# Optimization experiments

Measured on AMD Instinct MI355X. Metric: run time of the kernel, lower is better.

Reference implementation:

```python
import jax, jax.numpy as jnp
import numpy as np


def _conv2d(x, w, b):
    # x: [N,C,H,W], w: [O,I,kh,kw], valid conv, stride 1 (matches nn.Conv2d defaults)
    y = jax.lax.conv_general_dilated(
        x, w, window_strides=(1, 1), padding='VALID',
        dimension_numbers=('NCHW', 'OIHW', 'NCHW'))
    return y + b[None, :, None, None]


def _max_pool2(x):
    # F.max_pool2d(x, 2): 2x2 window, stride 2, no padding
    return jax.lax.reduce_window(
        x, -jnp.inf, jax.lax.max,
        window_dimensions=(1, 1, 2, 2), window_strides=(1, 1, 2, 2),
        padding='VALID')


def setup_inputs() -> dict:
    key = jax.random.key(0)
    ks = jax.random.split(key, 12)
    B = 16384
    def w(k, shape, fan_in):
        bound = 1.0 / np.sqrt(fan_in)
        return jax.random.uniform(k, shape, jnp.float32, -bound, bound)
    return {
        'x': jax.random.normal(ks[0], (B, 1, 28, 28), jnp.float32),
        'conv1_w': w(ks[1], (8, 1, 3, 3), 1 * 9),
        'conv1_b': w(ks[2], (8,), 1 * 9),
        'conv2_w': w(ks[3], (16, 8, 3, 3), 8 * 9),
        'conv2_b': w(ks[4], (16,), 8 * 9),
        'fc_w': w(ks[5], (128, 400), 400),
        'fc_b': w(ks[6], (128,), 400),
        'fc2_w': w(ks[7], (64, 128), 128),
        'fc2_b': w(ks[8], (64,), 128),
        'fc3_w': w(ks[9], (10, 64), 64),
        'fc3_b': w(ks[10], (10,), 64),
    }


def reference(x, conv1_w, conv1_b, conv2_w, conv2_b,
              fc_w, fc_b, fc2_w, fc2_b, fc3_w, fc3_b):
    out = jax.nn.relu(_conv2d(x, conv1_w, conv1_b))          # [B,8,26,26]
    out = _max_pool2(out)                                    # [B,8,13,13]
    out = jax.nn.relu(_conv2d(out, conv2_w, conv2_b))        # [B,16,11,11]
    out = _max_pool2(out)                                    # [B,16,5,5]
    out = out.reshape(out.shape[0], -1)                      # [B,400] (C,H,W order)
    out = jax.nn.relu(out @ fc_w.T + fc_b)                   # [B,128]
    out = out @ fc2_w.T + fc2_b                              # [B,64]
    out = out @ fc3_w.T + fc3_b                              # [B,10]
    return out
```

## Files before the change

kernel.cpp:

```cpp
#include <hip/hip_runtime.h>
#include <hip/hip_bf16.h>

typedef _Float16 half8 __attribute__((ext_vector_type(8)));
typedef float floatx4 __attribute__((ext_vector_type(4)));

__global__ __launch_bounds__(512, 4) void lenet_mfma(
    const float* __restrict__ X,
    const float* __restrict__ W1, const float* __restrict__ B1,
    const float* __restrict__ W2, const float* __restrict__ B2,
    const float* __restrict__ FW, const float* __restrict__ FB,
    const float* __restrict__ F2W, const float* __restrict__ F2B,
    const float* __restrict__ F3W, const float* __restrict__ F3B,
    float* __restrict__ OUT) {
  __shared__ __align__(16) _Float16 p2h[32 * 416];
  __shared__ __align__(16) char p1region[10816];
  __shared__ __align__(16) char region[20480];
  __shared__ __align__(16) _Float16 w2L[16 * 104];
  __shared__ float w1L[72];
  __shared__ float bc1L[8], bc2L[16], fbL[128], f2bL[64], f3bL[16];
  __shared__ __align__(16) _Float16 zero16[8];

  float* xs = (float*)region;
  _Float16* c2f = (_Float16*)region;
  _Float16* fwdb = (_Float16*)region;
  _Float16* w2sf = (_Float16*)region;
  float* w3sf = (float*)(region + 17408);
  _Float16* p1f = (_Float16*)p1region;
  float* h2f = (float*)p1region;
  _Float16* h1f = p2h;

  const int tid = threadIdx.x;
  const int wave = tid >> 6;
  const int lane = tid & 63;
  const int l15 = lane & 15;
  const int l4 = lane >> 4;
  const int m32 = blockIdx.x * 32;

  for (int i = tid; i < 72; i += 512) w1L[i] = W1[i];
  if (tid < 8) bc1L[tid] = B1[tid];
  if (tid >= 8 && tid < 24) bc2L[tid - 8] = B2[tid - 8];
  if (tid >= 32 && tid < 160) fbL[tid - 32] = FB[tid - 32];
  if (tid >= 160 && tid < 224) f2bL[tid - 160] = F2B[tid - 160];
  if (tid >= 224 && tid < 234) f3bL[tid - 224] = F3B[tid - 224];
  if (tid >= 240 && tid < 248) zero16[tid - 240] = (_Float16)0.f;
  for (int i = tid; i < 16 * 104; i += 512) {
    int oc = i / 104, k = i % 104;
    _Float16 v = (_Float16)0.f;
    if (k < 72) { int tap = k >> 3, ic = k & 7; v = (_Float16)W2[(oc * 8 + ic) * 9 + tap]; }
    w2L[i] = v;
  }
  if (tid < 512) { int rr = tid >> 4, cc = tid & 15; p2h[rr * 416 + 400 + cc] = (_Float16)0.f; }
  for (int i = tid; i < 784; i += 512) {
    int m = i / 196, f = i % 196;
    ((float4*)(xs + m * 784))[f] = ((const float4*)(X + (size_t)(m32 + m) * 784))[f];
  }
  __syncthreads();

  half8 bw0 = *(const half8*)(w2L + l15 * 104 + 0 + l4 * 8);
  half8 bw1 = *(const half8*)(w2L + l15 * 104 + 32 + l4 * 8);
  half8 bw2 = *(const half8*)(w2L + l15 * 104 + 64 + l4 * 8);
  int off0, off1, off2; int va0, va1, va2;
  {
    int tap, du, dv;
    tap = 0 * 4 + l4; du = (tap >= 6) ? 2 : ((tap >= 3) ? 1 : 0); dv = tap - 3 * du;
    off0 = (du * 13 + dv) * 16; va0 = (tap < 9);
    tap = 1 * 4 + l4; du = (tap >= 6) ? 2 : ((tap >= 3) ? 1 : 0); dv = tap - 3 * du;
    off1 = (du * 13 + dv) * 16; va1 = (tap < 9);
    tap = 2 * 4 + l4; du = (tap >= 6) ? 2 : ((tap >= 3) ? 1 : 0); dv = tap - 3 * du;
    off2 = (du * 13 + dv) * 16; va2 = (tap < 9);
  }

  for (int sb = 0; sb < 8; ++sb) {
    for (int t = tid; t < 416; t += 512) {
      int ch = t & 7, rm = t >> 3, m = rm / 13, r = rm % 13;
      float wk[9];
#pragma unroll
      for (int k = 0; k < 9; k++) wk[k] = w1L[ch * 9 + k];
      float b = bc1L[ch];
      const float* Xb = xs + m * 784 + 2 * r * 28;
      float2 A0[4], A1[4];
#pragma unroll
      for (int row = 0; row < 4; row++) {
        A0[row] = *(const float2*)(Xb + row * 28);
        A1[row] = *(const float2*)(Xb + row * 28 + 2);
      }
#pragma unroll
      for (int c = 0; c < 13; c++) {
        if (c) {
#pragma unroll
          for (int row = 0; row < 4; row++) {
            A0[row] = A1[row];
            A1[row] = *(const float2*)(Xb + row * 28 + 2 * c + 2);
          }
        }
        float s0 = 0.f, s1 = 0.f, s2 = 0.f, s3 = 0.f;
#pragma unroll
        for (int u = 0; u < 3; u++) {
          float w0 = wk[u * 3], w1 = wk[u * 3 + 1], w2v = wk[u * 3 + 2];
          float xu0 = A0[u].x, xu1 = A0[u].y, xu2 = A1[u].x, xu3 = A1[u].y;
          s0 += w0 * xu0 + w1 * xu1 + w2v * xu2;
          s1 += w0 * xu1 + w1 * xu2 + w2v * xu3;
          float xd0 = A0[u + 1].x, xd1 = A0[u + 1].y, xd2 = A1[u + 1].x, xd3 = A1[u + 1].y;
          s2 += w0 * xd0 + w1 * xd1 + w2v * xd2;
          s3 += w0 * xd1 + w1 * xd2 + w2v * xd3;
        }
        float mx = fmaxf(fmaxf(s0, s1), fmaxf(s2, s3));
        p1f[((m * 13 + r) * 13 + c) * 8 + ch] = (_Float16)fmaxf(mx + b, 0.f);
      }
    }
    __syncthreads();

    for (int mt = wave; mt < 31; mt += 8) {
      int p = mt * 16 + l15; if (p > 483) p = 483;
      int img = p / 121, rem = p - img * 121;
      int r = rem / 11, c = rem - r * 11;
      int base = ((img * 13 + r) * 13 + c) * 16;
      const char* p1c = (const char*)p1f;
      floatx4 acc = {0.f, 0.f, 0.f, 0.f};
      half8 a0 = *(const half8*)(va0 ? (p1c + base + off0) : (const char*)zero16);
      acc = __builtin_amdgcn_mfma_f32_16x16x32_f16(a0, bw0, acc, 0, 0, 0);
      half8 a1 = *(const half8*)(va1 ? (p1c + base + off1) : (const char*)zero16);
      acc = __builtin_amdgcn_mfma_f32_16x16x32_f16(a1, bw1, acc, 0, 0, 0);
      half8 a2 = *(const half8*)(va2 ? (p1c + base + off2) : (const char*)zero16);
      acc = __builtin_amdgcn_mfma_f32_16x16x32_f16(a2, bw2, acc, 0, 0, 0);
      int pb = mt * 16 + l4 * 4;
#pragma unroll
      for (int rr = 0; rr < 4; rr++) {
        int pos = pb + rr;
        if (pos < 484) c2f[pos * 16 + l15] = (_Float16)acc[rr];
      }
    }
    __syncthreads();

    for (int t = tid; t < 1600; t += 512) {
      int oc = t & 15, q = t >> 4;
      int m = q / 25, rc = q % 25, r = rc / 5, cc = rc % 5;
      int p00 = m * 121 + (2 * r) * 11 + 2 * cc;
      float v00 = (float)c2f[p00 * 16 + oc];
      float v01 = (float)c2f[(p00 + 1) * 16 + oc];
      float v10 = (float)c2f[(p00 + 11) * 16 + oc];
      float v11 = (float)c2f[(p00 + 12) * 16 + oc];
      float mx = fmaxf(fmaxf(v00, v01), fmaxf(v10, v11));
      p2h[(sb * 4 + m) * 416 + oc * 25 + r * 5 + cc] = (_Float16)fmaxf(mx + bc2L[oc], 0.f);
    }
    __syncthreads();
    if (sb < 7) {
      for (int i = tid; i < 784; i += 512) {
        int m = i / 196, f = i % 196;
        ((float4*)(xs + m * 784))[f] =
            ((const float4*)(X + (size_t)(m32 + (sb + 1) * 4 + m) * 784))[f];
      }
    }
    __syncthreads();
  }

  const int so = tid >> 2, sq = tid & 3;
  auto stageFW = [&](int c, int buf) {
    int kk = c * 32 + sq * 8;
    float4 z = {0.f, 0.f, 0.f, 0.f};
    float4 v0 = (kk < 400) ? *(const float4*)(FW + (size_t)so * 400 + kk) : z;
    float4 v1 = (kk + 4 < 400) ? *(const float4*)(FW + (size_t)so * 400 + kk + 4) : z;
    half8 h = {(_Float16)v0.x, (_Float16)v0.y, (_Float16)v0.z, (_Float16)v0.w,
               (_Float16)v1.x, (_Float16)v1.y, (_Float16)v1.z, (_Float16)v1.w};
    *(half8*)(fwdb + buf * 5120 + so * 40 + sq * 8) = h;
  };
  stageFW(0, 0);
  const int mt1 = wave & 1, nt0 = wave >> 1;
  floatx4 acc0 = {0.f, 0.f, 0.f, 0.f}, acc1 = {0.f, 0.f, 0.f, 0.f};
  for (int c = 0; c < 13; ++c) {
    __syncthreads();
    if (c < 12) stageFW(c + 1, (c + 1) & 1);
    const _Float16* fb = fwdb + (c & 1) * 5120;
    half8 a = *(const half8*)(p2h + (mt1 * 16 + l15) * 416 + c * 32 + l4 * 8);
    half8 b0 = *(const half8*)(fb + (nt0 * 16 + l15) * 40 + l4 * 8);
    half8 b1 = *(const half8*)(fb + ((nt0 + 4) * 16 + l15) * 40 + l4 * 8);
    acc0 = __builtin_amdgcn_mfma_f32_16x16x32_f16(a, b0, acc0, 0, 0, 0);
    acc1 = __builtin_amdgcn_mfma_f32_16x16x32_f16(a, b1, acc1, 0, 0, 0);
  }
  __syncthreads();

  {
    float bias0 = fbL[nt0 * 16 + l15], bias1 = fbL[(nt0 + 4) * 16 + l15];
#pragma unroll
    for (int rr = 0; rr < 4; rr++) {
      int img = mt1 * 16 + l4 * 4 + rr;
      h1f[img * 136 + nt0 * 16 + l15] = (_Float16)fmaxf(acc0[rr] + bias0, 0.f);
      h1f[img * 136 + (nt0 + 4) * 16 + l15] = (_Float16)fmaxf(acc1[rr] + bias1, 0.f);
    }
  }
  {
    int o = tid >> 3, q = tid & 7;
    const float* src = F2W + (size_t)o * 128 + q * 16;
    float4 v0 = *(const float4*)(src);
    float4 v1 = *(const float4*)(src + 4);
    float4 v2 = *(const float4*)(src + 8);
    float4 v3 = *(const float4*)(src + 12);
    half8 hA = {(_Float16)v0.x, (_Float16)v0.y, (_Float16)v0.z, (_Float16)v0.w,
                (_Float16)v1.x, (_Float16)v1.y, (_Float16)v1.z, (_Float16)v1.w};
    half8 hB = {(_Float16)v2.x, (_Float16)v2.y, (_Float16)v2.z, (_Float16)v2.w,
                (_Float16)v3.x, (_Float16)v3.y, (_Float16)v3.z, (_Float16)v3.w};
    *(half8*)(w2sf + o * 136 + q * 16) = hA;
    *(half8*)(w2sf + o * 136 + q * 16 + 8) = hB;
  }
  for (int i = tid; i < 640; i += 512) w3sf[(i >> 6) * 68 + (i & 63)] = F3W[i];
  __syncthreads();

  {
    floatx4 acc2 = {0.f, 0.f, 0.f, 0.f};
#pragma unroll
    for (int kt = 0; kt < 4; kt++) {
      half8 a = *(const half8*)(h1f + (mt1 * 16 + l15) * 136 + kt * 32 + l4 * 8);
      half8 b = *(const half8*)(w2sf + (nt0 * 16 + l15) * 136 + kt * 32 + l4 * 8);
      acc2 = __builtin_amdgcn_mfma_f32_16x16x32_f16(a, b, acc2, 0, 0, 0);
    }
    float b2v = f2bL[nt0 * 16 + l15];
#pragma unroll
    for (int rr = 0; rr < 4; rr++) {
      int img = mt1 * 16 + l4 * 4 + rr;
      h2f[img * 68 + nt0 * 16 + l15] = acc2[rr] + b2v;
    }
  }
  __syncthreads();

  {
    int img = tid >> 4, o = tid & 15;
    if (o < 10) {
      float s = f3bL[o];
#pragma unroll
      for (int k4 = 0; k4 < 16; k4++) {
        float4 hv = *(const float4*)(h2f + img * 68 + k4 * 4);
        float4 wv = *(const float4*)(w3sf + o * 68 + k4 * 4);
        s += hv.x * wv.x + hv.y * wv.y + hv.z * wv.z + hv.w * wv.w;
      }
      OUT[(size_t)(m32 + img) * 10 + o] = s;
    }
  }
}

extern "C" void kernel_launch(void* const* d_in, const int* in_sizes, int n_in,
                              void* d_out, int out_size, void* d_ws, size_t ws_size,
                              hipStream_t stream) {
  const float* x   = (const float*)d_in[0];
  const float* c1w = (const float*)d_in[1];
  const float* c1b = (const float*)d_in[2];
  const float* c2w = (const float*)d_in[3];
  const float* c2b = (const float*)d_in[4];
  const float* fw  = (const float*)d_in[5];
  const float* fb  = (const float*)d_in[6];
  const float* f2w = (const float*)d_in[7];
  const float* f2b = (const float*)d_in[8];
  const float* f3w = (const float*)d_in[9];
  const float* f3b = (const float*)d_in[10];
  float* out = (float*)d_out;

  const int B = in_sizes[0] / 784;
  lenet_mfma<<<B / 32, 512, 0, stream>>>(x, c1w, c1b, c2w, c2b,
                                         fw, fb, f2w, f2b, f3w, f3b, out);
}
```

Baseline: 153.6 us.

## Move conv1 to MFMA, fuse pools into conv epilogues, halve images per block

After: 136.2 us. -11.3%, faster.

```diff
diff --git a/kernel.cpp b/kernel.cpp
--- a/kernel.cpp
+++ b/kernel.cpp
@@ -4,7 +4,7 @@
 typedef _Float16 half8 __attribute__((ext_vector_type(8)));
 typedef float floatx4 __attribute__((ext_vector_type(4)));
 
-__global__ __launch_bounds__(512, 4) void lenet_mfma(
+__global__ __launch_bounds__(512, 8) void lenet_mfma2(
     const float* __restrict__ X,
     const float* __restrict__ W1, const float* __restrict__ B1,
     const float* __restrict__ W2, const float* __restrict__ B2,
@@ -12,54 +12,65 @@
     const float* __restrict__ F2W, const float* __restrict__ F2B,
     const float* __restrict__ F3W, const float* __restrict__ F3B,
     float* __restrict__ OUT) {
-  __shared__ __align__(16) _Float16 p2h[32 * 416];
-  __shared__ __align__(16) char p1region[10816];
-  __shared__ __align__(16) char region[20480];
+  __shared__ __align__(16) _Float16 p2h[16 * 424];
+  __shared__ __align__(16) char region[18944];
   __shared__ __align__(16) _Float16 w2L[16 * 104];
-  __shared__ float w1L[72];
+  __shared__ __align__(16) _Float16 c1B[1280];
   __shared__ float bc1L[8], bc2L[16], fbL[128], f2bL[64], f3bL[16];
   __shared__ __align__(16) _Float16 zero16[8];
 
-  float* xs = (float*)region;
-  _Float16* c2f = (_Float16*)region;
-  _Float16* fwdb = (_Float16*)region;
+  _Float16* xs = (_Float16*)region;
+  _Float16* p1f = (_Float16*)(region + 7168);
   _Float16* w2sf = (_Float16*)region;
-  float* w3sf = (float*)(region + 17408);
-  _Float16* p1f = (_Float16*)p1region;
-  float* h2f = (float*)p1region;
+  _Float16* w3sf = (_Float16*)(region + 17408);
   _Float16* h1f = p2h;
+  float* h2f = (float*)((char*)p2h + 6656);
 
   const int tid = threadIdx.x;
-  const int wave = tid >> 6;
-  const int lane = tid & 63;
-  const int l15 = lane & 15;
-  const int l4 = lane >> 4;
-  const int m32 = blockIdx.x * 32;
-
-  for (int i = tid; i < 72; i += 512) w1L[i] = W1[i];
+  const int wave = tid >> 6, lane = tid & 63, l15 = lane & 15, l4 = lane >> 4;
+  const int m16 = blockIdx.x * 16;
+  const float4* X4 = (const float4*)X;
+
   if (tid < 8) bc1L[tid] = B1[tid];
-  if (tid >= 8 && tid < 24) bc2L[tid - 8] = B2[tid - 8];
-  if (tid >= 32 && tid < 160) fbL[tid - 32] = FB[tid - 32];
-  if (tid >= 160 && tid < 224) f2bL[tid - 160] = F2B[tid - 160];
-  if (tid >= 224 && tid < 234) f3bL[tid - 224] = F3B[tid - 224];
-  if (tid >= 240 && tid < 248) zero16[tid - 240] = (_Float16)0.f;
-  for (int i = tid; i < 16 * 104; i += 512) {
+  else if (tid < 24) bc2L[tid - 8] = B2[tid - 8];
+  else if (tid < 152) fbL[tid - 24] = FB[tid - 24];
+  else if (tid < 216) f2bL[tid - 152] = F2B[tid - 152];
+  else if (tid < 226) f3bL[tid - 216] = F3B[tid - 216];
+  else if (tid >= 240 && tid < 248) zero16[tid - 240] = (_Float16)0.f;
+
+  for (int i = tid; i < 1664; i += 512) {
     int oc = i / 104, k = i % 104;
     _Float16 v = (_Float16)0.f;
     if (k < 72) { int tap = k >> 3, ic = k & 7; v = (_Float16)W2[(oc * 8 + ic) * 9 + tap]; }
     w2L[i] = v;
   }
-  if (tid < 512) { int rr = tid >> 4, cc = tid & 15; p2h[rr * 416 + 400 + cc] = (_Float16)0.f; }
+  for (int i = tid; i < 1280; i += 512) {
+    int mat = i / 640, r = i % 640, n = r / 40, k = r % 40;
+    float v = 0.f;
+    if (k < 16) {
+      int q = mat * 2 + (n >> 3), ch = n & 7;
+      int uu = (k >> 2) - (q >> 1), vv = (k & 3) - (q & 1);
+      if (uu >= 0 && uu < 3 && vv >= 0 && vv < 3) v = W1[ch * 9 + uu * 3 + vv];
+    }
+    c1B[i] = (_Float16)v;
+  }
+  if (tid < 384) { int rr = tid / 24; p2h[rr * 424 + 400 + tid % 24] = (_Float16)0.f; }
   for (int i = tid; i < 784; i += 512) {
-    int m = i / 196, f = i % 196;
-    ((float4*)(xs + m * 784))[f] = ((const float4*)(X + (size_t)(m32 + m) * 784))[f];
-  }
-  __syncthreads();
-
-  half8 bw0 = *(const half8*)(w2L + l15 * 104 + 0 + l4 * 8);
-  half8 bw1 = *(const half8*)(w2L + l15 * 104 + 32 + l4 * 8);
-  half8 bw2 = *(const half8*)(w2L + l15 * 104 + 64 + l4 * 8);
-  int off0, off1, off2; int va0, va1, va2;
+    int img = i / 196, f = i % 196, row = f / 7, fc = f % 7;
+    float4 v = X4[(size_t)(m16 + img) * 196 + f];
+    union { _Float16 h[4]; uint2 u; } pk;
+    pk.h[0] = (_Float16)v.x; pk.h[1] = (_Float16)v.y;
+    pk.h[2] = (_Float16)v.z; pk.h[3] = (_Float16)v.w;
+    *(uint2*)(xs + (img * 28 + row) * 32 + fc * 4) = pk.u;
+  }
+  __syncthreads();
+
+  const half8 cb0 = *(const half8*)(c1B + l15 * 40 + l4 * 8);
+  const half8 cb1 = *(const half8*)(c1B + 640 + l15 * 40 + l4 * 8);
+  const half8 bw0 = *(const half8*)(w2L + l15 * 104 + 0 + l4 * 8);
+  const half8 bw1 = *(const half8*)(w2L + l15 * 104 + 32 + l4 * 8);
+  const half8 bw2 = *(const half8*)(w2L + l15 * 104 + 64 + l4 * 8);
+  int off0, off1, off2, va0, va1, va2;
   {
     int tap, du, dv;
     tap = 0 * 4 + l4; du = (tap >= 6) ? 2 : ((tap >= 3) ? 1 : 0); dv = tap - 3 * du;
@@ -70,127 +81,64 @@
     off2 = (du * 13 + dv) * 16; va2 = (tap < 9);
   }
 
-  for (int sb = 0; sb < 8; ++sb) {
-    for (int t = tid; t < 416; t += 512) {
-      int ch = t & 7, rm = t >> 3, m = rm / 13, r = rm % 13;
-      float wk[9];
-#pragma unroll
-      for (int k = 0; k < 9; k++) wk[k] = w1L[ch * 9 + k];
-      float b = bc1L[ch];
-      const float* Xb = xs + m * 784 + 2 * r * 28;
-      float2 A0[4], A1[4];
-#pragma unroll
-      for (int row = 0; row < 4; row++) {
-        A0[row] = *(const float2*)(Xb + row * 28);
-        A1[row] = *(const float2*)(Xb + row * 28 + 2);
+  for (int sb = 0; sb < 4; ++sb) {
+    for (int mt = wave; mt < 43; mt += 8) {
+      int m = mt * 16 + l15; if (m > 675) m = 675;
+      int img = m / 169, rem = m - img * 169, wr = rem / 13, wc = rem - wr * 13;
+      int rowa = img * 28 + 2 * wr + 2 * l4; if (rowa > 110) rowa = 110;
+      const uint32_t* xd = (const uint32_t*)xs;
+      int dw = rowa * 16 + wc;
+      union { uint32_t u[4]; half8 h; } ua;
+      ua.u[0] = xd[dw]; ua.u[1] = xd[dw + 1];
+      ua.u[2] = xd[dw + 16]; ua.u[3] = xd[dw + 17];
+      floatx4 ac1 = {0.f, 0.f, 0.f, 0.f}, ac2 = {0.f, 0.f, 0.f, 0.f};
+      ac1 = __builtin_amdgcn_mfma_f32_16x16x32_f16(ua.h, cb0, ac1, 0, 0, 0);
+      ac2 = __builtin_amdgcn_mfma_f32_16x16x32_f16(ua.h, cb1, ac2, 0, 0, 0);
+#pragma unroll
+      for (int rr = 0; rr < 4; ++rr) {
+        float mx = fmaxf(ac1[rr], ac2[rr]);
+        mx = fmaxf(mx, __shfl_xor(mx, 8));
+        int w = mt * 16 + 4 * l4 + rr;
+        if (l15 < 8 && w < 676) {
+          int wi = w / 169, wrem = w - wi * 169, pr = wrem / 13, pcc = wrem - pr * 13;
+          p1f[(wi * 169 + pr * 13 + pcc) * 8 + l15] = (_Float16)fmaxf(mx + bc1L[l15], 0.f);
+        }
       }
-#pragma unroll
-      for (int c = 0; c < 13; c++) {
-        if (c) {
-#pragma unroll
-          for (int row = 0; row < 4; row++) {
-            A0[row] = A1[row];
-            A1[row] = *(const float2*)(Xb + row * 28 + 2 * c + 2);
-          }
-        }
-        float s0 = 0.f, s1 = 0.f, s2 = 0.f, s3 = 0.f;
-#pragma unroll
-        for (int u = 0; u < 3; u++) {
-          float w0 = wk[u * 3], w1 = wk[u * 3 + 1], w2v = wk[u * 3 + 2];
-          float xu0 = A0[u].x, xu1 = A0[u].y, xu2 = A1[u].x, xu3 = A1[u].y;
-          s0 += w0 * xu0 + w1 * xu1 + w2v * xu2;
-          s1 += w0 * xu1 + w1 * xu2 + w2v * xu3;
-          float xd0 = A0[u + 1].x, xd1 = A0[u + 1].y, xd2 = A1[u + 1].x, xd3 = A1[u + 1].y;
-          s2 += w0 * xd0 + w1 * xd1 + w2v * xd2;
-          s3 += w0 * xd1 + w1 * xd2 + w2v * xd3;
-        }
-        float mx = fmaxf(fmaxf(s0, s1), fmaxf(s2, s3));
-        p1f[((m * 13 + r) * 13 + c) * 8 + ch] = (_Float16)fmaxf(mx + b, 0.f);
+    }
+    __syncthreads();
+    for (int mt = wave; mt < 25; mt += 8) {
+      int w = mt * 4 + (l15 >> 2), q = l15 & 3;
+      int img = w / 25, rem = w - img * 25, wr = rem / 5, wc = rem - wr * 5;
+      int r = 2 * wr + (q >> 1), c = 2 * wc + (q & 1);
+      const char* pbase = (const char*)p1f;
+      int base = (img * 169 + r * 13 + c) * 16;
+      floatx4 acc = {0.f, 0.f, 0.f, 0.f};
+      half8 a0 = *(const half8*)(va0 ? pbase + base + off0 : (const char*)zero16);
+      acc = __builtin_amdgcn_mfma_f32_16x16x32_f16(a0, bw0, acc, 0, 0, 0);
+      half8 a1 = *(const half8*)(va1 ? pbase + base + off1 : (const char*)zero16);
+      acc = __builtin_amdgcn_mfma_f32_16x16x32_f16(a1, bw1, acc, 0, 0, 0);
+      half8 a2 = *(const half8*)(va2 ? pbase + base + off2 : (const char*)zero16);
+      acc = __builtin_amdgcn_mfma_f32_16x16x32_f16(a2, bw2, acc, 0, 0, 0);
+      float mx = fmaxf(fmaxf(acc[0], acc[1]), fmaxf(acc[2], acc[3]));
+      int w2 = mt * 4 + l4, i2 = w2 / 25, rm2 = w2 - i2 * 25, wr2 = rm2 / 5, wc2 = rm2 - wr2 * 5;
+      p2h[(sb * 4 + i2) * 424 + l15 * 25 + wr2 * 5 + wc2] = (_Float16)fmaxf(mx + bc2L[l15], 0.f);
+    }
+    if (sb < 3) {
+      for (int i = tid; i < 784; i += 512) {
+        int img = i / 196, f = i % 196, row = f / 7, fc = f % 7;
+        float4 v = X4[(size_t)(m16 + (sb + 1) * 4 + img) * 196 + f];
+        union { _Float16 h[4]; uint2 u; } pk;
+        pk.h[0] = (_Float16)v.x; pk.h[1] = (_Float16)v.y;
+        pk.h[2] = (_Float16)v.z; pk.h[3] = (_Float16)v.w;
+        *(uint2*)(xs + (img * 28 + row) * 32 + fc * 4) = pk.u;
       }
     }
     __syncthreads();
-
-    for (int mt = wave; mt < 31; mt += 8) {
-      int p = mt * 16 + l15; if (p > 483) p = 483;
-      int img = p / 121, rem = p - img * 121;
-      int r = rem / 11, c = rem - r * 11;
-      int base = ((img * 13 + r) * 13 + c) * 16;
-      const char* p1c = (const char*)p1f;
-      floatx4 acc = {0.f, 0.f, 0.f, 0.f};
-      half8 a0 = *(const half8*)(va0 ? (p1c + base + off0) : (const char*)zero16);
-      acc = __builtin_amdgcn_mfma_f32_16x16x32_f16(a0, bw0, acc, 0, 0, 0);
-      half8 a1 = *(const half8*)(va1 ? (p1c + base + off1) : (const char*)zero16);
-      acc = __builtin_amdgcn_mfma_f32_16x16x32_f16(a1, bw1, acc, 0, 0, 0);
-      half8 a2 = *(const half8*)(va2 ? (p1c + base + off2) : (const char*)zero16);
-      acc = __builtin_amdgcn_mfma_f32_16x16x32_f16(a2, bw2, acc, 0, 0, 0);
-      int pb = mt * 16 + l4 * 4;
-#pragma unroll
-      for (int rr = 0; rr < 4; rr++) {
-        int pos = pb + rr;
-        if (pos < 484) c2f[pos * 16 + l15] = (_Float16)acc[rr];
-      }
-    }
-    __syncthreads();
-
-    for (int t = tid; t < 1600; t += 512) {
-      int oc = t & 15, q = t >> 4;
-      int m = q / 25, rc = q % 25, r = rc / 5, cc = rc % 5;
-      int p00 = m * 121 + (2 * r) * 11 + 2 * cc;
-      float v00 = (float)c2f[p00 * 16 + oc];
-      float v01 = (float)c2f[(p00 + 1) * 16 + oc];
-      float v10 = (float)c2f[(p00 + 11) * 16 + oc];
-      float v11 = (float)c2f[(p00 + 12) * 16 + oc];
-      float mx = fmaxf(fmaxf(v00, v01), fmaxf(v10, v11));
-      p2h[(sb * 4 + m) * 416 + oc * 25 + r * 5 + cc] = (_Float16)fmaxf(mx + bc2L[oc], 0.f);
-    }
-    __syncthreads();
-    if (sb < 7) {
-      for (int i = tid; i < 784; i += 512) {
-        int m = i / 196, f = i % 196;
-        ((float4*)(xs + m * 784))[f] =
-            ((const float4*)(X + (size_t)(m32 + (sb + 1) * 4 + m) * 784))[f];
-      }
-    }
-    __syncthreads();
-  }
-
-  const int so = tid >> 2, sq = tid & 3;
-  auto stageFW = [&](int c, int buf) {
-    int kk = c * 32 + sq * 8;
-    float4 z = {0.f, 0.f, 0.f, 0.f};
-    float4 v0 = (kk < 400) ? *(const float4*)(FW + (size_t)so * 400 + kk) : z;
-    float4 v1 = (kk + 4 < 400) ? *(const float4*)(FW + (size_t)so * 400 + kk + 4) : z;
-    half8 h = {(_Float16)v0.x, (_Float16)v0.y, (_Float16)v0.z, (_Float16)v0.w,
-               (_Float16)v1.x, (_Float16)v1.y, (_Float16)v1.z, (_Float16)v1.w};
-    *(half8*)(fwdb + buf * 5120 + so * 40 + sq * 8) = h;
-  };
-  stageFW(0, 0);
-  const int mt1 = wave & 1, nt0 = wave >> 1;
-  floatx4 acc0 = {0.f, 0.f, 0.f, 0.f}, acc1 = {0.f, 0.f, 0.f, 0.f};
-  for (int c = 0; c < 13; ++c) {
-    __syncthreads();
-    if (c < 12) stageFW(c + 1, (c + 1) & 1);
-    const _Float16* fb = fwdb + (c & 1) * 5120;
-    half8 a = *(const half8*)(p2h + (mt1 * 16 + l15) * 416 + c * 32 + l4 * 8);
-    half8 b0 = *(const half8*)(fb + (nt0 * 16 + l15) * 40 + l4 * 8);
-    half8 b1 = *(const half8*)(fb + ((nt0 + 4) * 16 + l15) * 40 + l4 * 8);
-    acc0 = __builtin_amdgcn_mfma_f32_16x16x32_f16(a, b0, acc0, 0, 0, 0);
-    acc1 = __builtin_amdgcn_mfma_f32_16x16x32_f16(a, b1, acc1, 0, 0, 0);
-  }
-  __syncthreads();
+  }
 
   {
-    float bias0 = fbL[nt0 * 16 + l15], bias1 = fbL[(nt0 + 4) * 16 + l15];
-#pragma unroll
-    for (int rr = 0; rr < 4; rr++) {
-      int img = mt1 * 16 + l4 * 4 + rr;
-      h1f[img * 136 + nt0 * 16 + l15] = (_Float16)fmaxf(acc0[rr] + bias0, 0.f);
-      h1f[img * 136 + (nt0 + 4) * 16 + l15] = (_Float16)fmaxf(acc1[rr] + bias1, 0.f);
-    }
-  }
-  {
-    int o = tid >> 3, q = tid & 7;
-    const float* src = F2W + (size_t)o * 128 + q * 16;
+    int o = tid >> 3, qq = tid & 7;
+    const float* src = F2W + (size_t)o * 128 + qq * 16;
     float4 v0 = *(const float4*)(src);
     float4 v1 = *(const float4*)(src + 4);
     float4 v2 = *(const float4*)(src + 8);
@@ -199,41 +147,75 @@
                 (_Float16)v1.x, (_Float16)v1.y, (_Float16)v1.z, (_Float16)v1.w};
     half8 hB = {(_Float16)v2.x, (_Float16)v2.y, (_Float16)v2.z, (_Float16)v2.w,
                 (_Float16)v3.x, (_Float16)v3.y, (_Float16)v3.z, (_Float16)v3.w};
-    *(half8*)(w2sf + o * 136 + q * 16) = hA;
-    *(half8*)(w2sf + o * 136 + q * 16 + 8) = hB;
-  }
-  for (int i = tid; i < 640; i += 512) w3sf[(i >> 6) * 68 + (i & 63)] = F3W[i];
-  __syncthreads();
-
+    *(half8*)(w2sf + o * 136 + qq * 16) = hA;
+    *(half8*)(w2sf + o * 136 + qq * 16 + 8) = hB;
+  }
+  if (tid < 80) {
+    int o = tid / 8, qq = tid & 7;
+    const float* src = F3W + o * 64 + qq * 8;
+    float4 v0 = *(const float4*)(src);
+    float4 v1 = *(const float4*)(src + 4);
+    half8 h = {(_Float16)v0.x, (_Float16)v0.y, (_Float16)v0.z, (_Float16)v0.w,
+               (_Float16)v1.x, (_Float16)v1.y, (_Float16)v1.z, (_Float16)v1.w};
+    *(half8*)(w3sf + o * 72 + qq * 8) = h;
+  }
+
+  const int o1 = wave * 16 + l15;
+  const float4* FWq = (const float4*)FW;
+  const float4 fz = {0.f, 0.f, 0.f, 0.f};
+  float4 cur0, cur1, nxt0, nxt1;
+  { int kn = l4 * 8;
+    cur0 = FWq[(size_t)o1 * 100 + (kn >> 2)];
+    cur1 = FWq[(size_t)o1 * 100 + (kn >> 2) + 1]; }
+  floatx4 fa = {0.f, 0.f, 0.f, 0.f};
+  for (int c = 0; c < 13; ++c) {
+    if (c < 12) {
+      int kn = (c + 1) * 32 + l4 * 8;
+      nxt0 = (kn < 400) ? FWq[(size_t)o1 * 100 + (kn >> 2)] : fz;
+      nxt1 = (kn + 4 < 400) ? FWq[(size_t)o1 * 100 + (kn >> 2) + 1] : fz;
+    }
+    half8 a = *(const half8*)(p2h + l15 * 424 + c * 32 + l4 * 8);
+    half8 b = {(_Float16)cur0.x, (_Float16)cur0.y, (_Float16)cur0.z, (_Float16)cur0.w,
+               (_Float16)cur1.x, (_Float16)cur1.y, (_Float16)cur1.z, (_Float16)cur1.w};
+    fa = __builtin_amdgcn_mfma_f32_16x16x32_f16(a, b, fa, 0, 0, 0);
+    cur0 = nxt0; cur1 = nxt1;
+  }
+  __syncthreads();
   {
-    floatx4 acc2 = {0.f, 0.f, 0.f, 0.f};
-#pragma unroll
-    for (int kt = 0; kt < 4; kt++) {
-      half8 a = *(const half8*)(h1f + (mt1 * 16 + l15) * 136 + kt * 32 + l4 * 8);
-      half8 b = *(const half8*)(w2sf + (nt0 * 16 + l15) * 136 + kt * 32 + l4 * 8);
-      acc2 = __builtin_amdgcn_mfma_f32_16x16x32_f16(a, b, acc2, 0, 0, 0);
-    }
-    float b2v = f2bL[nt0 * 16 + l15];
-#pragma unroll
-    for (int rr = 0; rr < 4; rr++) {
-      int img = mt1 * 16 + l4 * 4 + rr;
-      h2f[img * 68 + nt0 * 16 + l15] = acc2[rr] + b2v;
-    }
-  }
-  __syncthreads();
-
-  {
-    int img = tid >> 4, o = tid & 15;
-    if (o < 10) {
-      float s = f3bL[o];
-#pragma unroll
-      for (int k4 = 0; k4 < 16; k4++) {
-        float4 hv = *(const float4*)(h2f + img * 68 + k4 * 4);
-        float4 wv = *(const float4*)(w3sf + o * 68 + k4 * 4);
-        s += hv.x * wv.x + hv.y * wv.y + hv.z * wv.z + hv.w * wv.w;
-      }
-      OUT[(size_t)(m32 + img) * 10 + o] = s;
-    }
+    float bia = fbL[o1];
+#pragma unroll
+    for (int rr = 0; rr < 4; ++rr)
+      h1f[(4 * l4 + rr) * 136 + o1] = (_Float16)fmaxf(fa[rr] + bia, 0.f);
+  }
+  __syncthreads();
+
+  if (wave < 4) {
+    floatx4 a2 = {0.f, 0.f, 0.f, 0.f};
+#pragma unroll
+    for (int kt = 0; kt < 4; ++kt) {
+      half8 a = *(const half8*)(h1f + l15 * 136 + kt * 32 + l4 * 8);
+      half8 b = *(const half8*)(w2sf + (wave * 16 + l15) * 136 + kt * 32 + l4 * 8);
+      a2 = __builtin_amdgcn_mfma_f32_16x16x32_f16(a, b, a2, 0, 0, 0);
+    }
+    float bb = f2bL[wave * 16 + l15];
+#pragma unroll
+    for (int rr = 0; rr < 4; ++rr)
+      h2f[(4 * l4 + rr) * 68 + wave * 16 + l15] = a2[rr] + bb;
+  }
+  __syncthreads();
+
+  if (tid < 160) {
+    int img = tid / 10, o = tid - img * 10;
+    float s = f3bL[o];
+#pragma unroll
+    for (int kc = 0; kc < 8; ++kc) {
+      half8 wv = *(const half8*)(w3sf + o * 72 + kc * 8);
+      float4 hA = *(const float4*)(h2f + img * 68 + kc * 8);
+      float4 hB = *(const float4*)(h2f + img * 68 + kc * 8 + 4);
+      s += hA.x * (float)wv[0] + hA.y * (float)wv[1] + hA.z * (float)wv[2] + hA.w * (float)wv[3]
+         + hB.x * (float)wv[4] + hB.y * (float)wv[5] + hB.z * (float)wv[6] + hB.w * (float)wv[7];
+    }
+    OUT[(size_t)(m16 + img) * 10 + o] = s;
   }
 }
 
@@ -254,6 +236,6 @@
   float* out = (float*)d_out;
 
   const int B = in_sizes[0] / 784;
-  lenet_mfma<<<B / 32, 512, 0, stream>>>(x, c1w, c1b, c2w, c2b,
-                                         fw, fb, f2w, f2b, f3w, f3b, out);
+  lenet_mfma2<<<B / 16, 512, 0, stream>>>(x, c1w, c1b, c2w, c2b,
+                                          fw, fb, f2w, f2b, f3w, f3b, out);
 }
```
